# Kernel tuning notes

Measured on AMD Instinct MI355X. Metric: run time of the kernel, lower is better.

## Reference

```python
import jax, jax.numpy as jnp
import numpy as np

B, S, HID = 1, 4096, 1024
H, KV, D = 16, 4, 64           # heads, kv heads, head_dim
N_REP = H // KV
WINDOW = 512
EPS = 1e-5
ROPE_THETA = 1e6


def _rope_tables(seq_len, dim, theta):
    inv_freq = 1.0 / (theta ** (np.arange(0, dim, 2, dtype=np.float32) / dim))
    t = np.arange(seq_len, dtype=np.float32)
    freqs = np.outer(t, inv_freq)                      # [S, D/2]
    emb = np.concatenate([freqs, freqs], axis=-1)      # [S, D]
    return jnp.asarray(np.cos(emb)), jnp.asarray(np.sin(emb))


def setup_inputs() -> dict:
    key = jax.random.key(0)
    ks = jax.random.split(key, 7)
    cos, sin = _rope_tables(S, D, ROPE_THETA)
    return {
        "x": jax.random.normal(ks[0], (B, S, HID), jnp.float32),
        "cos": cos,
        "sin": sin,
        "wq": jax.random.normal(ks[1], (H * D, HID), jnp.float32) * (HID ** -0.5),
        "wk": jax.random.normal(ks[2], (KV * D, HID), jnp.float32) * (HID ** -0.5),
        "wv": jax.random.normal(ks[3], (KV * D, HID), jnp.float32) * (HID ** -0.5),
        "wo": jax.random.normal(ks[4], (HID, H * D), jnp.float32) * (HID ** -0.5),
        "q_norm_w": jnp.ones((D,), jnp.float32),
        "k_norm_w": jnp.ones((D,), jnp.float32),
        "sinks": jax.random.normal(ks[5], (H,), jnp.float32),
    }


def _rms_norm(v, w):
    return v * jax.lax.rsqrt(jnp.mean(v * v, axis=-1, keepdims=True) + EPS) * w


def _rotate_half(v):
    h = v.shape[-1] // 2
    return jnp.concatenate([-v[..., h:], v[..., :h]], axis=-1)


def reference(x, cos, sin, wq, wk, wv, wo, q_norm_w, k_norm_w, sinks):
    b, s, _ = x.shape
    q = (x @ wq.T).reshape(b, s, H, D)
    k = (x @ wk.T).reshape(b, s, KV, D)
    v = (x @ wv.T).reshape(b, s, KV, D)
    q = _rms_norm(q, q_norm_w)
    k = _rms_norm(k, k_norm_w)
    c = cos[:, None, :]  # [s,1,d] broadcast over heads
    sn = sin[:, None, :]
    q = q * c + _rotate_half(q) * sn
    k = k * c + _rotate_half(k) * sn
    # GQA: repeat kv heads
    k = jnp.repeat(k, N_REP, axis=2)  # [b,s,H,D]
    v = jnp.repeat(v, N_REP, axis=2)
    scores = jnp.einsum("bqhd,bkhd->bhqk", q, k) / np.sqrt(D)  # [b,H,s,s]
    i = jnp.arange(s)[:, None]
    j = jnp.arange(s)[None, :]
    allowed = (j <= i) & (j > i - WINDOW)  # causal + sliding window
    scores = jnp.where(allowed, scores, -jnp.inf)
    # append per-head learned sink logit, softmax in fp32, then drop sink col
    sink = jnp.broadcast_to(sinks.reshape(1, H, 1, 1), (b, H, s, 1))
    attn = jax.nn.softmax(jnp.concatenate([scores, sink], axis=-1).astype(jnp.float32), axis=-1)
    attn = attn[..., :-1].astype(q.dtype)
    out = jnp.einsum("bhqk,bkhd->bqhd", attn, v).reshape(b, s, H * D)
    return out @ wo.T
```

## Files before the change

kernel.cpp:

```cpp
#include <hip/hip_runtime.h>
#include <hip/hip_bf16.h>
#include <stdint.h>

#define S_LEN   4096
#define HIDDEN  1024
#define NHEAD   16
#define NKV     4
#define HD      64
#define WINDOW  512
#define L2E     1.4426950408889634f
#define QSCALE  (0.125f * L2E)

using short8 = __attribute__((ext_vector_type(8))) short;
using f32x4  = __attribute__((ext_vector_type(4))) float;

__device__ __forceinline__ uint16_t f2bf(float f) {
  uint32_t u = __builtin_bit_cast(uint32_t, f);
  u += 0x7fffu + ((u >> 16) & 1u);
  return (uint16_t)(u >> 16);
}
__device__ __forceinline__ uint16_t f2bf_rn(float f) {
  uint32_t u = __builtin_bit_cast(uint32_t, f);
  return (uint16_t)((u + 0x8000u) >> 16);
}
__device__ __forceinline__ uint32_t pk2(float a, float b) {
  return (uint32_t)f2bf_rn(a) | ((uint32_t)f2bf_rn(b) << 16);
}

__device__ __forceinline__ void gld_lds16(void* lds, const void* g) {
  __builtin_amdgcn_global_load_lds(
      (const __attribute__((address_space(1))) char*)g,
      (__attribute__((address_space(3))) char*)lds, 16, 0, 0);
}

__global__ __launch_bounds__(256) void k_tobf16(
    const float* __restrict__ x, const float* __restrict__ wq,
    const float* __restrict__ wk, const float* __restrict__ wv,
    const float* __restrict__ wo,
    uint16_t* __restrict__ xb, uint16_t* __restrict__ wqkvb,
    uint16_t* __restrict__ wob) {
  int i = blockIdx.x * 256 + threadIdx.x;
  const float4* src; uint16_t* dst; int off;
  if (i < 1048576)      { src = (const float4*)x;  dst = xb;                off = i; }
  else if (i < 1310720) { src = (const float4*)wq; dst = wqkvb;             off = i - 1048576; }
  else if (i < 1376256) { src = (const float4*)wk; dst = wqkvb + 1024*1024; off = i - 1310720; }
  else if (i < 1441792) { src = (const float4*)wv; dst = wqkvb + 1280*1024; off = i - 1376256; }
  else                  { src = (const float4*)wo; dst = wob;               off = i - 1441792; }
  float4 v = src[off];
  ushort4 o = { f2bf(v.x), f2bf(v.y), f2bf(v.z), f2bf(v.w) };
  *(ushort4*)(dst + (size_t)off * 4) = o;
}

__global__ __launch_bounds__(256) void k_gemm_qkv(
    const uint16_t* __restrict__ A, const uint16_t* __restrict__ B,
    const float* __restrict__ cosb, const float* __restrict__ sinb,
    const float* __restrict__ qw, const float* __restrict__ kw,
    uint16_t* __restrict__ qout, uint16_t* __restrict__ kout,
    uint16_t* __restrict__ vtout) {
  __shared__ uint16_t As[64 * 64];
  __shared__ uint16_t Bs[128 * 64];
  const int K = 1024;
  const int t = threadIdx.x;
  const int lane = t & 63, w = t >> 6;
  const int wr = w >> 1, wc = w & 1;
  const int l16 = lane & 15, lg = lane >> 4;
  const int bid = blockIdx.x;
  const int xcd = bid & 7, idx = bid >> 3;
  const int bm = xcd + 8 * (idx & 7);
  const int bn = idx >> 3;
  const uint16_t* Ab = A + (size_t)bm * 64 * K;
  const uint16_t* Bb = B + (size_t)bn * 128 * K;
  f32x4 acc[2][4] = {};
  for (int k0 = 0; k0 < K; k0 += 64) {
    __syncthreads();
    {
      int row = t >> 3, c8 = (t & 7) << 3;
      gld_lds16(&As[t * 8], Ab + (size_t)row * K + k0 + c8);
      int t2 = t + 256, row2 = t2 >> 3, c82 = (t2 & 7) << 3;
      gld_lds16(&As[t2 * 8], Ab + (size_t)row2 * K + k0 + c82);
    }
#pragma unroll
    for (int it = 0; it < 4; ++it) {
      int idx2 = it * 256 + t;
      int row = idx2 >> 3, c8 = (idx2 & 7) << 3;
      gld_lds16(&Bs[idx2 * 8], Bb + (size_t)row * K + k0 + c8);
    }
    __syncthreads();
#pragma unroll
    for (int kk = 0; kk < 2; ++kk) {
      short8 af[2], bq[4];
#pragma unroll
      for (int i = 0; i < 2; ++i)
        af[i] = *(const short8*)&As[(wr * 32 + i * 16 + l16) * 64 + kk * 32 + lg * 8];
#pragma unroll
      for (int j = 0; j < 4; ++j)
        bq[j] = *(const short8*)&Bs[(wc * 64 + j * 16 + l16) * 64 + kk * 32 + lg * 8];
#pragma unroll
      for (int i = 0; i < 2; ++i)
#pragma unroll
        for (int j = 0; j < 4; ++j)
          acc[i][j] = __builtin_amdgcn_mfma_f32_16x16x32_bf16(af[i], bq[j], acc[i][j], 0, 0, 0);
    }
  }

  const int hg = bn * 2 + wc;
  if (hg >= 20) {
    const int kvh = hg - 20;
#pragma unroll
    for (int i = 0; i < 2; ++i) {
      int row0 = bm * 64 + wr * 32 + i * 16 + lg * 4;
#pragma unroll
      for (int j = 0; j < 4; ++j) {
        int d = j * 16 + l16;
        ushort4 o = { f2bf(acc[i][j][0]), f2bf(acc[i][j][1]),
                      f2bf(acc[i][j][2]), f2bf(acc[i][j][3]) };
        *(ushort4*)(vtout + (size_t)(kvh * 64 + d) * S_LEN + row0) = o;
      }
    }
    return;
  }
  const float* nw = (hg < 16) ? qw : kw;
  float wgt[4];
#pragma unroll
  for (int j = 0; j < 4; ++j) wgt[j] = nw[j * 16 + l16];
#pragma unroll
  for (int i = 0; i < 2; ++i) {
    int row0 = bm * 64 + wr * 32 + i * 16 + lg * 4;
    float qn[4][4];
#pragma unroll
    for (int r = 0; r < 4; ++r) {
      float ss = acc[i][0][r] * acc[i][0][r] + acc[i][1][r] * acc[i][1][r]
               + acc[i][2][r] * acc[i][2][r] + acc[i][3][r] * acc[i][3][r];
      ss += __shfl_xor(ss, 1);
      ss += __shfl_xor(ss, 2);
      ss += __shfl_xor(ss, 4);
      ss += __shfl_xor(ss, 8);
      float inv = rsqrtf(ss * (1.0f / 64.0f) + 1e-5f);
#pragma unroll
      for (int j = 0; j < 4; ++j) qn[j][r] = acc[i][j][r] * inv * wgt[j];
    }
#pragma unroll
    for (int j = 0; j < 4; ++j) {
      int d = j * 16 + l16;
#pragma unroll
      for (int r = 0; r < 4; ++r) {
        int row = row0 + r;
        float rot = (j < 2) ? -qn[j + 2][r] : qn[j - 2][r];
        float o = qn[j][r] * cosb[row * 64 + d] + rot * sinb[row * 64 + d];
        if (hg < 16)
          qout[(size_t)row * HIDDEN + hg * 64 + d] = f2bf(o * QSCALE);
        else
          kout[((size_t)(hg - 16) * S_LEN + row) * 64 + d] = f2bf(o);
      }
    }
  }
}

__global__ __launch_bounds__(256) void k_gemm_bf16(
    const uint16_t* __restrict__ A, const uint16_t* __restrict__ B,
    float* __restrict__ C, int N, int K) {
  __shared__ uint16_t As[64 * 64];
  __shared__ uint16_t Bs[128 * 64];
  const int t = threadIdx.x;
  const int lane = t & 63, w = t >> 6;
  const int wr = w >> 1, wc = w & 1;
  const int l16 = lane & 15, lg = lane >> 4;
  const int bid = blockIdx.x;
  const int xcd = bid & 7, idx = bid >> 3;
  const int bm = xcd + 8 * (idx & 7);
  const int bn = idx >> 3;
  const uint16_t* Ab = A + (size_t)bm * 64 * K;
  const uint16_t* Bb = B + (size_t)bn * 128 * K;
  f32x4 acc[2][4] = {};
  for (int k0 = 0; k0 < K; k0 += 64) {
    __syncthreads();
    {
      int row = t >> 3, c8 = (t & 7) << 3;
      gld_lds16(&As[t * 8], Ab + (size_t)row * K + k0 + c8);
      int t2 = t + 256, row2 = t2 >> 3, c82 = (t2 & 7) << 3;
      gld_lds16(&As[t2 * 8], Ab + (size_t)row2 * K + k0 + c82);
    }
#pragma unroll
    for (int it = 0; it < 4; ++it) {
      int idx2 = it * 256 + t;
      int row = idx2 >> 3, c8 = (idx2 & 7) << 3;
      gld_lds16(&Bs[idx2 * 8], Bb + (size_t)row * K + k0 + c8);
    }
    __syncthreads();
#pragma unroll
    for (int kk = 0; kk < 2; ++kk) {
      short8 af[2], bq[4];
#pragma unroll
      for (int i = 0; i < 2; ++i)
        af[i] = *(const short8*)&As[(wr * 32 + i * 16 + l16) * 64 + kk * 32 + lg * 8];
#pragma unroll
      for (int j = 0; j < 4; ++j)
        bq[j] = *(const short8*)&Bs[(wc * 64 + j * 16 + l16) * 64 + kk * 32 + lg * 8];
#pragma unroll
      for (int i = 0; i < 2; ++i)
#pragma unroll
        for (int j = 0; j < 4; ++j)
          acc[i][j] = __builtin_amdgcn_mfma_f32_16x16x32_bf16(af[i], bq[j], acc[i][j], 0, 0, 0);
    }
  }
#pragma unroll
  for (int i = 0; i < 2; ++i) {
    int row0 = bm * 64 + wr * 32 + i * 16 + lg * 4;
#pragma unroll
    for (int j = 0; j < 4; ++j) {
      int col = bn * 128 + wc * 64 + j * 16 + l16;
#pragma unroll
      for (int r = 0; r < 4; ++r)
        C[(size_t)(row0 + r) * N + col] = acc[i][j][r];
    }
  }
}

__global__ __launch_bounds__(512) void k_attn(
    const uint16_t* __restrict__ qb,
    const uint16_t* __restrict__ kb,
    const uint16_t* __restrict__ vtb,
    const float* __restrict__ sinks,
    uint16_t* __restrict__ ao) {
  __shared__ uint16_t Kl[64][72];
  __shared__ uint16_t Vl[64][72];
  __shared__ uint16_t Pl[8][16][72];
  const int bid = blockIdx.x;
  const int hp = bid & 7;
  const int q0 = (63 - (bid >> 3)) * 64;
  const int kvh = hp >> 1;
  const int t = threadIdx.x;
  const int lane = t & 63, w = t >> 6;
  const int h = kvh * 4 + (hp & 1) * 2 + (w >> 2);
  const int wq = w & 3;
  const int l16 = lane & 15, lg = lane >> 4;
  const int qrow = q0 + wq * 16 + l16;

  short8 bq0, bq1;
  {
    const uint16_t* qp = qb + (size_t)qrow * HIDDEN + h * 64 + lg * 8;
    bq0 = *(const short8*)qp;
    bq1 = *(const short8*)(qp + 32);
  }
  float lsum = 0.f;
  f32x4 acc[4] = {};

  int kstart = q0 - WINDOW;
  if (kstart < 0) kstart = 0;

  const int srow = t >> 3, sc8 = (t & 7) << 3;
  const uint16_t* kp = kb + ((size_t)kvh * S_LEN + srow) * 64 + sc8;
  const uint16_t* vp = vtb + ((size_t)kvh * 64 + srow) * S_LEN + sc8;
  short8 nk = *(const short8*)(kp + (size_t)kstart * 64);
  short8 nv = *(const short8*)(vp + kstart);

  for (int k0 = kstart; k0 <= q0; k0 += 64) {
    __syncthreads();
    *(short8*)&Kl[srow][sc8] = nk;
    *(short8*)&Vl[srow][sc8] = nv;
    __syncthreads();
    if (k0 + 64 <= q0) {
      nk = *(const short8*)(kp + (size_t)(k0 + 64) * 64);
      nv = *(const short8*)(vp + k0 + 64);
    }

    f32x4 st[4] = {};
    __builtin_amdgcn_s_setprio(1);
#pragma unroll
    for (int c = 0; c < 4; ++c) {
      short8 ak0 = *(const short8*)&Kl[c * 16 + l16][lg * 8];
      short8 ak1 = *(const short8*)&Kl[c * 16 + l16][32 + lg * 8];
      st[c] = __builtin_amdgcn_mfma_f32_16x16x32_bf16(ak0, bq0, st[c], 0, 0, 0);
      st[c] = __builtin_amdgcn_mfma_f32_16x16x32_bf16(ak1, bq1, st[c], 0, 0, 0);
    }
    __builtin_amdgcn_s_setprio(0);

    float p[4][4];
    if (k0 == q0 || k0 == q0 - WINDOW) {
#pragma unroll
      for (int c = 0; c < 4; ++c) {
        int keyb = k0 + c * 16 + lg * 4;
#pragma unroll
        for (int r = 0; r < 4; ++r) {
          int key = keyb + r;
          bool ok = (key <= qrow) && (key + WINDOW > qrow);
          p[c][r] = ok ? exp2f(st[c][r]) : 0.f;
        }
      }
    } else {
#pragma unroll
      for (int c = 0; c < 4; ++c)
#pragma unroll
        for (int r = 0; r < 4; ++r)
          p[c][r] = exp2f(st[c][r]);
    }
#pragma unroll
    for (int c = 0; c < 4; ++c)
      lsum += (p[c][0] + p[c][1]) + (p[c][2] + p[c][3]);

#pragma unroll
    for (int c = 0; c < 4; ++c) {
      uint2 pw = { pk2(p[c][0], p[c][1]), pk2(p[c][2], p[c][3]) };
      *(uint2*)&Pl[w][l16][c * 16 + lg * 4] = pw;
    }
    asm volatile("s_waitcnt lgkmcnt(0)" ::: "memory");
    short8 pa0 = *(const short8*)&Pl[w][l16][lg * 8];
    short8 pa1 = *(const short8*)&Pl[w][l16][32 + lg * 8];
    __builtin_amdgcn_s_setprio(1);
#pragma unroll
    for (int dt = 0; dt < 4; ++dt) {
      short8 bv0 = *(const short8*)&Vl[dt * 16 + l16][lg * 8];
      short8 bv1 = *(const short8*)&Vl[dt * 16 + l16][32 + lg * 8];
      acc[dt] = __builtin_amdgcn_mfma_f32_16x16x32_bf16(pa0, bv0, acc[dt], 0, 0, 0);
      acc[dt] = __builtin_amdgcn_mfma_f32_16x16x32_bf16(pa1, bv1, acc[dt], 0, 0, 0);
    }
    __builtin_amdgcn_s_setprio(0);
  }

  lsum += __shfl_xor(lsum, 16);
  lsum += __shfl_xor(lsum, 32);
  float sk = exp2f(sinks[h] * L2E);
  float inv = 1.0f / (lsum + sk);
#pragma unroll
  for (int r = 0; r < 4; ++r) {
    float rd = __shfl(inv, lg * 4 + r);
    int row = q0 + wq * 16 + lg * 4 + r;
#pragma unroll
    for (int dt = 0; dt < 4; ++dt)
      ao[(size_t)row * HIDDEN + h * 64 + dt * 16 + l16] = f2bf(acc[dt][r] * rd);
  }
}

extern "C" void kernel_launch(void* const* d_in, const int* in_sizes, int n_in,
                              void* d_out, int out_size, void* d_ws, size_t ws_size,
                              hipStream_t stream) {
  const float* x     = (const float*)d_in[0];
  const float* cosb  = (const float*)d_in[1];
  const float* sinb  = (const float*)d_in[2];
  const float* wq    = (const float*)d_in[3];
  const float* wk    = (const float*)d_in[4];
  const float* wv    = (const float*)d_in[5];
  const float* wo    = (const float*)d_in[6];
  const float* qnw   = (const float*)d_in[7];
  const float* knw   = (const float*)d_in[8];
  const float* sinks = (const float*)d_in[9];
  float* out = (float*)d_out;

  char* ws = (char*)d_ws;
  uint16_t* xb    = (uint16_t*)(ws);
  uint16_t* wqkvb = (uint16_t*)(ws + (8ll  << 20));
  uint16_t* wob   = (uint16_t*)(ws + (11ll << 20));
  uint16_t* qsc   = (uint16_t*)(ws + (13ll << 20));
  uint16_t* kbf   = (uint16_t*)(ws + (21ll << 20));
  uint16_t* vtb   = (uint16_t*)(ws + (23ll << 20));
  uint16_t* aob   = (uint16_t*)(ws + (25ll << 20));

  k_tobf16  <<<6656, 256, 0, stream>>>(x, wq, wk, wv, wo, xb, wqkvb, wob);
  k_gemm_qkv<<<768, 256, 0, stream>>>(xb, wqkvb, cosb, sinb, qnw, knw,
                                      qsc, kbf, vtb);
  k_attn    <<<512, 512, 0, stream>>>(qsc, kbf, vtb, sinks, aob);
  k_gemm_bf16<<<512, 256, 0, stream>>>(aob, wob, out, 1024, 1024);
}
```

Baseline: 81.13 us.

## Double-buffer attention K/V tiles via direct global-to-LDS loads with XOR swizzle

The attention kernel now stages K and V tiles into two LDS buffers using direct global-to-LDS loads (gld_lds16) instead of loading into registers and then storing to LDS. The next tile is prefetched into the alternate buffer while the current one is computed, and one barrier per iteration replaces the two. The padded rows give way to an XOR column swizzle to avoid LDS bank conflicts without padding. The risk is that correctness depends on the async loads finishing before the barrier, which needs a vmcnt wait that may or may not sit inside gld_lds16.

```diff
diff --git a/kernel.cpp b/kernel.cpp
--- a/kernel.cpp
+++ b/kernel.cpp
@@ -222,8 +222,8 @@
     const uint16_t* __restrict__ vtb,
     const float* __restrict__ sinks,
     uint16_t* __restrict__ ao) {
-  __shared__ uint16_t Kl[64][72];
-  __shared__ uint16_t Vl[64][72];
+  __shared__ uint16_t Kl[2][64][64];
+  __shared__ uint16_t Vl[2][64][64];
   __shared__ uint16_t Pl[8][16][72];
   const int bid = blockIdx.x;
   const int hp = bid & 7;
@@ -235,6 +235,7 @@
   const int wq = w & 3;
   const int l16 = lane & 15, lg = lane >> 4;
   const int qrow = q0 + wq * 16 + l16;
+  const int sw = l16 & 7;
 
   short8 bq0, bq1;
   {
@@ -248,28 +249,28 @@
   int kstart = q0 - WINDOW;
   if (kstart < 0) kstart = 0;
 
-  const int srow = t >> 3, sc8 = (t & 7) << 3;
-  const uint16_t* kp = kb + ((size_t)kvh * S_LEN + srow) * 64 + sc8;
-  const uint16_t* vp = vtb + ((size_t)kvh * 64 + srow) * S_LEN + sc8;
-  short8 nk = *(const short8*)(kp + (size_t)kstart * 64);
-  short8 nv = *(const short8*)(vp + kstart);
-
-  for (int k0 = kstart; k0 <= q0; k0 += 64) {
-    __syncthreads();
-    *(short8*)&Kl[srow][sc8] = nk;
-    *(short8*)&Vl[srow][sc8] = nv;
-    __syncthreads();
+  const int srow = t >> 3;
+  const int scol = ((t & 7) ^ (srow & 7)) << 3;
+  const uint16_t* kp = kb + ((size_t)kvh * S_LEN + srow) * 64 + scol;
+  const uint16_t* vp = vtb + ((size_t)kvh * 64 + srow) * S_LEN + scol;
+
+  gld_lds16(&Kl[0][0][0] + (size_t)t * 8, kp + (size_t)kstart * 64);
+  gld_lds16(&Vl[0][0][0] + (size_t)t * 8, vp + kstart);
+  __syncthreads();
+
+  int ib = 0;
+  for (int k0 = kstart; k0 <= q0; k0 += 64, ib ^= 1) {
     if (k0 + 64 <= q0) {
-      nk = *(const short8*)(kp + (size_t)(k0 + 64) * 64);
-      nv = *(const short8*)(vp + k0 + 64);
+      gld_lds16(&Kl[ib ^ 1][0][0] + (size_t)t * 8, kp + (size_t)(k0 + 64) * 64);
+      gld_lds16(&Vl[ib ^ 1][0][0] + (size_t)t * 8, vp + k0 + 64);
     }
 
     f32x4 st[4] = {};
     __builtin_amdgcn_s_setprio(1);
 #pragma unroll
     for (int c = 0; c < 4; ++c) {
-      short8 ak0 = *(const short8*)&Kl[c * 16 + l16][lg * 8];
-      short8 ak1 = *(const short8*)&Kl[c * 16 + l16][32 + lg * 8];
+      short8 ak0 = *(const short8*)&Kl[ib][c * 16 + l16][(lg ^ sw) * 8];
+      short8 ak1 = *(const short8*)&Kl[ib][c * 16 + l16][((lg + 4) ^ sw) * 8];
       st[c] = __builtin_amdgcn_mfma_f32_16x16x32_bf16(ak0, bq0, st[c], 0, 0, 0);
       st[c] = __builtin_amdgcn_mfma_f32_16x16x32_bf16(ak1, bq1, st[c], 0, 0, 0);
     }
@@ -309,12 +310,14 @@
     __builtin_amdgcn_s_setprio(1);
 #pragma unroll
     for (int dt = 0; dt < 4; ++dt) {
-      short8 bv0 = *(const short8*)&Vl[dt * 16 + l16][lg * 8];
-      short8 bv1 = *(const short8*)&Vl[dt * 16 + l16][32 + lg * 8];
+      short8 bv0 = *(const short8*)&Vl[ib][dt * 16 + l16][(lg ^ sw) * 8];
+      short8 bv1 = *(const short8*)&Vl[ib][dt * 16 + l16][((lg + 4) ^ sw) * 8];
       acc[dt] = __builtin_amdgcn_mfma_f32_16x16x32_bf16(pa0, bv0, acc[dt], 0, 0, 0);
       acc[dt] = __builtin_amdgcn_mfma_f32_16x16x32_bf16(pa1, bv1, acc[dt], 0, 0, 0);
     }
     __builtin_amdgcn_s_setprio(0);
+
+    __syncthreads();
   }
 
   lsum += __shfl_xor(lsum, 16);
```

After: 81.02 us, median of 2. Within noise of the previous version (-0.1%).

## Double GEMM K-tile depth and split attention blocks to one head each

Applied to the files above, without the earlier changes.

Both GEMM kernels now stage 128-wide K slices in LDS instead of 64, halving the number of barrier-separated iterations at the cost of larger shared memory (48KB per block). The attention kernel changes from 512-thread blocks covering two heads to 256-thread blocks covering one head, launched as 1024 blocks, with each thread loading two K/V rows per tile. This trades per-block K/V tile reuse across two heads for more, smaller blocks and possibly better occupancy. The P staging buffer shrinks to match.

```diff
diff --git a/kernel.cpp b/kernel.cpp
--- a/kernel.cpp
+++ b/kernel.cpp
@@ -57,8 +57,8 @@
     const float* __restrict__ qw, const float* __restrict__ kw,
     uint16_t* __restrict__ qout, uint16_t* __restrict__ kout,
     uint16_t* __restrict__ vtout) {
-  __shared__ uint16_t As[64 * 64];
-  __shared__ uint16_t Bs[128 * 64];
+  __shared__ uint16_t As[64 * 128];
+  __shared__ uint16_t Bs[128 * 128];
   const int K = 1024;
   const int t = threadIdx.x;
   const int lane = t & 63, w = t >> 6;
@@ -71,30 +71,30 @@
   const uint16_t* Ab = A + (size_t)bm * 64 * K;
   const uint16_t* Bb = B + (size_t)bn * 128 * K;
   f32x4 acc[2][4] = {};
-  for (int k0 = 0; k0 < K; k0 += 64) {
-    __syncthreads();
-    {
-      int row = t >> 3, c8 = (t & 7) << 3;
-      gld_lds16(&As[t * 8], Ab + (size_t)row * K + k0 + c8);
-      int t2 = t + 256, row2 = t2 >> 3, c82 = (t2 & 7) << 3;
-      gld_lds16(&As[t2 * 8], Ab + (size_t)row2 * K + k0 + c82);
-    }
+  for (int k0 = 0; k0 < K; k0 += 128) {
+    __syncthreads();
 #pragma unroll
     for (int it = 0; it < 4; ++it) {
-      int idx2 = it * 256 + t;
-      int row = idx2 >> 3, c8 = (idx2 & 7) << 3;
-      gld_lds16(&Bs[idx2 * 8], Bb + (size_t)row * K + k0 + c8);
-    }
-    __syncthreads();
-#pragma unroll
-    for (int kk = 0; kk < 2; ++kk) {
+      int id2 = it * 256 + t;
+      int row = id2 >> 4, c8 = (id2 & 15) << 3;
+      gld_lds16(&As[id2 * 8], Ab + (size_t)row * K + k0 + c8);
+    }
+#pragma unroll
+    for (int it = 0; it < 8; ++it) {
+      int id2 = it * 256 + t;
+      int row = id2 >> 4, c8 = (id2 & 15) << 3;
+      gld_lds16(&Bs[id2 * 8], Bb + (size_t)row * K + k0 + c8);
+    }
+    __syncthreads();
+#pragma unroll
+    for (int kk = 0; kk < 4; ++kk) {
       short8 af[2], bq[4];
 #pragma unroll
       for (int i = 0; i < 2; ++i)
-        af[i] = *(const short8*)&As[(wr * 32 + i * 16 + l16) * 64 + kk * 32 + lg * 8];
+        af[i] = *(const short8*)&As[(wr * 32 + i * 16 + l16) * 128 + kk * 32 + lg * 8];
 #pragma unroll
       for (int j = 0; j < 4; ++j)
-        bq[j] = *(const short8*)&Bs[(wc * 64 + j * 16 + l16) * 64 + kk * 32 + lg * 8];
+        bq[j] = *(const short8*)&Bs[(wc * 64 + j * 16 + l16) * 128 + kk * 32 + lg * 8];
 #pragma unroll
       for (int i = 0; i < 2; ++i)
 #pragma unroll
@@ -159,8 +159,8 @@
 __global__ __launch_bounds__(256) void k_gemm_bf16(
     const uint16_t* __restrict__ A, const uint16_t* __restrict__ B,
     float* __restrict__ C, int N, int K) {
-  __shared__ uint16_t As[64 * 64];
-  __shared__ uint16_t Bs[128 * 64];
+  __shared__ uint16_t As[64 * 128];
+  __shared__ uint16_t Bs[128 * 128];
   const int t = threadIdx.x;
   const int lane = t & 63, w = t >> 6;
   const int wr = w >> 1, wc = w & 1;
@@ -172,30 +172,30 @@
   const uint16_t* Ab = A + (size_t)bm * 64 * K;
   const uint16_t* Bb = B + (size_t)bn * 128 * K;
   f32x4 acc[2][4] = {};
-  for (int k0 = 0; k0 < K; k0 += 64) {
-    __syncthreads();
-    {
-      int row = t >> 3, c8 = (t & 7) << 3;
-      gld_lds16(&As[t * 8], Ab + (size_t)row * K + k0 + c8);
-      int t2 = t + 256, row2 = t2 >> 3, c82 = (t2 & 7) << 3;
-      gld_lds16(&As[t2 * 8], Ab + (size_t)row2 * K + k0 + c82);
-    }
+  for (int k0 = 0; k0 < K; k0 += 128) {
+    __syncthreads();
 #pragma unroll
     for (int it = 0; it < 4; ++it) {
-      int idx2 = it * 256 + t;
-      int row = idx2 >> 3, c8 = (idx2 & 7) << 3;
-      gld_lds16(&Bs[idx2 * 8], Bb + (size_t)row * K + k0 + c8);
-    }
-    __syncthreads();
-#pragma unroll
-    for (int kk = 0; kk < 2; ++kk) {
+      int id2 = it * 256 + t;
+      int row = id2 >> 4, c8 = (id2 & 15) << 3;
+      gld_lds16(&As[id2 * 8], Ab + (size_t)row * K + k0 + c8);
+    }
+#pragma unroll
+    for (int it = 0; it < 8; ++it) {
+      int id2 = it * 256 + t;
+      int row = id2 >> 4, c8 = (id2 & 15) << 3;
+      gld_lds16(&Bs[id2 * 8], Bb + (size_t)row * K + k0 + c8);
+    }
+    __syncthreads();
+#pragma unroll
+    for (int kk = 0; kk < 4; ++kk) {
       short8 af[2], bq[4];
 #pragma unroll
       for (int i = 0; i < 2; ++i)
-        af[i] = *(const short8*)&As[(wr * 32 + i * 16 + l16) * 64 + kk * 32 + lg * 8];
+        af[i] = *(const short8*)&As[(wr * 32 + i * 16 + l16) * 128 + kk * 32 + lg * 8];
 #pragma unroll
       for (int j = 0; j < 4; ++j)
-        bq[j] = *(const short8*)&Bs[(wc * 64 + j * 16 + l16) * 64 + kk * 32 + lg * 8];
+        bq[j] = *(const short8*)&Bs[(wc * 64 + j * 16 + l16) * 128 + kk * 32 + lg * 8];
 #pragma unroll
       for (int i = 0; i < 2; ++i)
 #pragma unroll
@@ -216,7 +216,7 @@
   }
 }
 
-__global__ __launch_bounds__(512) void k_attn(
+__global__ __launch_bounds__(256) void k_attn(
     const uint16_t* __restrict__ qb,
     const uint16_t* __restrict__ kb,
     const uint16_t* __restrict__ vtb,
@@ -224,17 +224,15 @@
     uint16_t* __restrict__ ao) {
   __shared__ uint16_t Kl[64][72];
   __shared__ uint16_t Vl[64][72];
-  __shared__ uint16_t Pl[8][16][72];
+  __shared__ uint16_t Pl[4][16][72];
   const int bid = blockIdx.x;
-  const int hp = bid & 7;
-  const int q0 = (63 - (bid >> 3)) * 64;
-  const int kvh = hp >> 1;
+  const int h = bid & 15;
+  const int q0 = (63 - (bid >> 4)) * 64;
+  const int kvh = h >> 2;
   const int t = threadIdx.x;
   const int lane = t & 63, w = t >> 6;
-  const int h = kvh * 4 + (hp & 1) * 2 + (w >> 2);
-  const int wq = w & 3;
   const int l16 = lane & 15, lg = lane >> 4;
-  const int qrow = q0 + wq * 16 + l16;
+  const int qrow = q0 + w * 16 + l16;
 
   short8 bq0, bq1;
   {
@@ -248,20 +246,28 @@
   int kstart = q0 - WINDOW;
   if (kstart < 0) kstart = 0;
 
-  const int srow = t >> 3, sc8 = (t & 7) << 3;
-  const uint16_t* kp = kb + ((size_t)kvh * S_LEN + srow) * 64 + sc8;
-  const uint16_t* vp = vtb + ((size_t)kvh * 64 + srow) * S_LEN + sc8;
-  short8 nk = *(const short8*)(kp + (size_t)kstart * 64);
-  short8 nv = *(const short8*)(vp + kstart);
+  const int r1 = t >> 3, sc8 = (t & 7) << 3;
+  const uint16_t* kp  = kb + ((size_t)kvh * S_LEN + r1) * 64 + sc8;
+  const uint16_t* kp2 = kp + (size_t)32 * 64;
+  const uint16_t* vp  = vtb + ((size_t)kvh * 64 + r1) * S_LEN + sc8;
+  const uint16_t* vp2 = vp + (size_t)32 * S_LEN;
+  short8 nk0 = *(const short8*)(kp  + (size_t)kstart * 64);
+  short8 nk1 = *(const short8*)(kp2 + (size_t)kstart * 64);
+  short8 nv0 = *(const short8*)(vp  + kstart);
+  short8 nv1 = *(const short8*)(vp2 + kstart);
 
   for (int k0 = kstart; k0 <= q0; k0 += 64) {
     __syncthreads();
-    *(short8*)&Kl[srow][sc8] = nk;
-    *(short8*)&Vl[srow][sc8] = nv;
+    *(short8*)&Kl[r1][sc8]      = nk0;
+    *(short8*)&Kl[r1 + 32][sc8] = nk1;
+    *(short8*)&Vl[r1][sc8]      = nv0;
+    *(short8*)&Vl[r1 + 32][sc8] = nv1;
     __syncthreads();
     if (k0 + 64 <= q0) {
-      nk = *(const short8*)(kp + (size_t)(k0 + 64) * 64);
-      nv = *(const short8*)(vp + k0 + 64);
+      nk0 = *(const short8*)(kp  + (size_t)(k0 + 64) * 64);
+      nk1 = *(const short8*)(kp2 + (size_t)(k0 + 64) * 64);
+      nv0 = *(const short8*)(vp  + k0 + 64);
+      nv1 = *(const short8*)(vp2 + k0 + 64);
     }
 
     f32x4 st[4] = {};
@@ -324,7 +330,7 @@
 #pragma unroll
   for (int r = 0; r < 4; ++r) {
     float rd = __shfl(inv, lg * 4 + r);
-    int row = q0 + wq * 16 + lg * 4 + r;
+    int row = q0 + w * 16 + lg * 4 + r;
 #pragma unroll
     for (int dt = 0; dt < 4; ++dt)
       ao[(size_t)row * HIDDEN + h * 64 + dt * 16 + l16] = f2bf(acc[dt][r] * rd);
@@ -358,6 +364,6 @@
   k_tobf16  <<<6656, 256, 0, stream>>>(x, wq, wk, wv, wo, xb, wqkvb, wob);
   k_gemm_qkv<<<768, 256, 0, stream>>>(xb, wqkvb, cosb, sinb, qnw, knw,
                                       qsc, kbf, vtb);
-  k_attn    <<<512, 512, 0, stream>>>(qsc, kbf, vtb, sinks, aob);
+  k_attn    <<<1024, 256, 0, stream>>>(qsc, kbf, vtb, sinks, aob);
   k_gemm_bf16<<<512, 256, 0, stream>>>(aob, wob, out, 1024, 1024);
 }
```

New measurement: 110.0 us. 35.6% more time.
